# Optimization experiments

Hardware: AMD Instinct MI355X
Metric: run time of the kernel (lower is better)

Reference implementation:

```python
import jax, jax.numpy as jnp
import numpy as np

# Static config matching init_kwargs
DIM, HEADS = 128, 4
WH, WW = 4, 32          # window size (h, w)
SH, SW = 2, 2           # shift size (h, w)
H, W, B = 64, 512, 8
N = WH * WW             # tokens per window = 128
HD = DIM // HEADS       # head dim = 32
SCALE = HD ** -0.5
NHW, NWW = H // WH, W // WW
NWIN = NHW * NWW


def _rel_pos_index():
    coords = np.stack(np.meshgrid(np.arange(WH), np.arange(WW), indexing='ij'))  # (2,WH,WW)
    flat = coords.reshape(2, -1)                      # (2,N)
    rel = (flat[:, :, None] - flat[:, None, :]).transpose(1, 2, 0)  # (N,N,2)
    rel[:, :, 0] += WH - 1
    rel[:, :, 1] += WW - 1
    rel[:, :, 0] *= 2 * WW - 1
    return rel.sum(-1)                                # (N,N) int


def _attn_mask():
    img = np.zeros((H, W))
    cnt = 0
    for h in (slice(0, -WH), slice(-WH, -SH), slice(-SH, None)):
        for w in (slice(0, -WW), slice(-WW, -SW), slice(-SW, None)):
            img[h, w] = cnt
            cnt += 1
    mw = img.reshape(NHW, WH, NWW, WW).transpose(0, 2, 1, 3).reshape(-1, N)  # (nW,N)
    diff = mw[:, None, :] - mw[:, :, None]            # (nW,N,N)
    return np.where(diff != 0, -100.0, 0.0).astype(np.float32)


_RPI = _rel_pos_index()
_MASK = _attn_mask()


def _layernorm(x, g, b):
    m = jnp.mean(x, axis=-1, keepdims=True)
    v = jnp.mean(jnp.square(x - m), axis=-1, keepdims=True)
    return (x - m) * jax.lax.rsqrt(v + 1e-5) * g + b


def setup_inputs() -> dict:
    key = jax.random.key(0)
    ks = jax.random.split(key, 6)
    s = 0.02
    return {
        'x': jax.random.normal(ks[0], (B, H, W, DIM), jnp.float32),
        'g1': jnp.ones((DIM,), jnp.float32),
        'b1': jnp.zeros((DIM,), jnp.float32),
        'qkv_w': jax.random.normal(ks[1], (DIM, 3 * DIM), jnp.float32) * s,
        'qkv_b': jnp.zeros((3 * DIM,), jnp.float32),
        'rpb': jax.random.normal(ks[2], ((2 * WH - 1) * (2 * WW - 1), HEADS), jnp.float32) * s,
        'proj_w': jax.random.normal(ks[3], (DIM, DIM), jnp.float32) * s,
        'proj_b': jnp.zeros((DIM,), jnp.float32),
        'g2': jnp.ones((DIM,), jnp.float32),
        'b2': jnp.zeros((DIM,), jnp.float32),
        'fc1_w': jax.random.normal(ks[4], (DIM, 4 * DIM), jnp.float32) * s,
        'fc1_b': jnp.zeros((4 * DIM,), jnp.float32),
        'fc2_w': jax.random.normal(ks[5], (4 * DIM, DIM), jnp.float32) * s,
        'fc2_b': jnp.zeros((DIM,), jnp.float32),
    }


def reference(x, g1, b1, qkv_w, qkv_b, rpb, proj_w, proj_b, g2, b2,
              fc1_w, fc1_b, fc2_w, fc2_b):
    mask = jnp.asarray(_MASK)                         # (nW,N,N)
    # ---- W-MSA branch ----
    y = _layernorm(x, g1, b1)
    y = jnp.roll(y, (-SH, -SW), axis=(1, 2))          # cyclic shift
    # window partition: (B,H,W,C) -> (B*nW, N, C)
    xw = y.reshape(B, NHW, WH, NWW, WW, DIM).transpose(0, 1, 3, 2, 4, 5)
    xw = xw.reshape(B * NWIN, N, DIM)
    qkv = (xw @ qkv_w + qkv_b).reshape(B * NWIN, N, 3, HEADS, HD)
    qkv = qkv.transpose(2, 0, 3, 1, 4)                # (3, B_, h, N, d)
    q, k, v = qkv[0] * SCALE, qkv[1], qkv[2]
    attn = jnp.einsum('bhid,bhjd->bhij', q, k)        # (B_, h, N, N)
    bias = rpb[_RPI.reshape(-1)].reshape(N, N, HEADS).transpose(2, 0, 1)
    attn = attn + bias[None]
    attn = attn.reshape(B, NWIN, HEADS, N, N) + mask[None, :, None]
    attn = jax.nn.softmax(attn.reshape(B * NWIN, HEADS, N, N), axis=-1)
    o = jnp.einsum('bhij,bhjd->bhid', attn, v)        # (B_, h, N, d)
    o = o.transpose(0, 2, 1, 3).reshape(B * NWIN, N, DIM)
    o = o @ proj_w + proj_b
    # window reverse + reverse shift
    o = o.reshape(B, NHW, NWW, WH, WW, DIM).transpose(0, 1, 3, 2, 4, 5)
    o = o.reshape(B, H, W, DIM)
    o = jnp.roll(o, (SH, SW), axis=(1, 2))
    x = x + o
    # ---- MLP branch ----
    z = _layernorm(x, g2, b2)
    z = jax.nn.gelu(z @ fc1_w + fc1_b, approximate=False) @ fc2_w + fc2_b
    return x + z
```

## Files before the change

kernel.cpp:

```cpp
#include <hip/hip_runtime.h>
#include <hip/hip_bf16.h>
#include <math.h>

constexpr int BATCH = 8;
constexpr int IMG_H = 64;
constexpr int IMG_W = 512;
constexpr int DIM   = 128;
constexpr int WIN_H = 4, WIN_W = 32;
constexpr int SHIFT_H = 2, SHIFT_W = 2;
constexpr int NTOK = 128;
constexpr int HEADS = 4, HD = 32;
constexpr float QK_SCALE = 0.17677669529663687f;

typedef __attribute__((ext_vector_type(8))) short bf16x8;
typedef __attribute__((ext_vector_type(4))) float f32x4;

__device__ __forceinline__ unsigned short f2bf(float f) {
    unsigned u = __float_as_uint(f);
    u = (u + 0x7fffu + ((u >> 16) & 1u)) >> 16;
    return (unsigned short)u;
}

__device__ __forceinline__ int sc(int r, int c) {
    return (r << 7) + (c ^ ((r & 7) << 3));
}

__device__ __forceinline__ float gelu_tanh(float v) {
    const float u = v * (0.7978845608028654f + 0.035677408136300125f * v * v);
    const float e = exp2f(u * -2.8853900817779268f);
    return v * __builtin_amdgcn_rcpf(1.0f + e);
}

__global__ __launch_bounds__(256) void prep_weights(
    const float* __restrict__ fc1_w, const float* __restrict__ fc2_w,
    const float* __restrict__ qkv_w, const float* __restrict__ proj_w,
    unsigned short* __restrict__ w1t, unsigned short* __restrict__ w2t,
    unsigned short* __restrict__ qkv_wt, unsigned short* __restrict__ proj_wt)
{
    const int tid = blockIdx.x * 256 + threadIdx.x;
    if (tid < 512 * 128) {
        const int n = tid >> 7, k = tid & 127;
        w1t[tid] = f2bf(fc1_w[k * 512 + n]);
    } else if (tid < 2 * 512 * 128) {
        const int t = tid - 512 * 128;
        const int n = t >> 9, k = t & 511;
        w2t[t] = f2bf(fc2_w[k * 128 + n]);
    } else if (tid < 2 * 512 * 128 + 384 * 128) {
        const int t = tid - 2 * 512 * 128;
        const int n = t >> 7, k = t & 127;
        float v = qkv_w[k * 384 + n];
        if (n < 128) v *= QK_SCALE;
        qkv_wt[t] = f2bf(v);
    } else if (tid < 2 * 512 * 128 + 384 * 128 + 128 * 128) {
        const int t = tid - (2 * 512 * 128 + 384 * 128);
        const int n = t >> 7, k = t & 127;
        proj_wt[t] = f2bf(proj_w[k * 128 + n]);
    }
}

__global__ __launch_bounds__(512, 2) void swin_attn_mfma(
    const float* __restrict__ x,
    const float* __restrict__ g1,
    const float* __restrict__ b1,
    const unsigned short* __restrict__ qkv_wt,
    const float* __restrict__ qkv_b,
    const float* __restrict__ rpb,
    const unsigned short* __restrict__ proj_wt,
    const float* __restrict__ proj_b,
    float* __restrict__ out)
{
    __shared__ __align__(16) unsigned short s_xw[128 * 128];
    __shared__ __align__(16) unsigned short s_q [128 * 128];
    __shared__ __align__(16) unsigned short s_k [128 * 128];
    __shared__ __align__(16) unsigned short s_vt[128 * 128];
    __shared__ float s_rpb[441 * 4];

    const int tid = threadIdx.x;
    const int wv  = tid >> 6;
    const int ln  = tid & 63;
    const int g   = ln >> 4;
    const int c15 = ln & 15;
    const int kq  = g * 8;
    const int qr0 = wv * 16;

    const int b   = blockIdx.x >> 8;
    const int wid = blockIdx.x & 255;
    const int wp  = wid >> 4;
    const int wq  = wid & 15;

    {
        const int lh = ln & 31;
        const int hf = ln >> 5;
        const float4 gv = *(const float4*)&g1[lh * 4];
        const float4 bv = *(const float4*)&b1[lh * 4];
        #pragma unroll
        for (int it = 0; it < 8; ++it) {
            const int t  = qr0 + it * 2 + hf;
            const int th = t >> 5, tw = t & 31;
            const int gh = (wp * WIN_H + th + SHIFT_H) & (IMG_H - 1);
            const int gw = (wq * WIN_W + tw + SHIFT_W) & (IMG_W - 1);
            const float4 v = *(const float4*)&x[((((size_t)b * IMG_H + gh) * IMG_W + gw) * DIM) + lh * 4];
            float s  = v.x + v.y + v.z + v.w;
            float s2 = v.x * v.x + v.y * v.y + v.z * v.z + v.w * v.w;
            #pragma unroll
            for (int off = 1; off < 32; off <<= 1) {
                s  += __shfl_xor(s, off);
                s2 += __shfl_xor(s2, off);
            }
            const float mean = s * (1.0f / 128.0f);
            const float rs   = rsqrtf(s2 * (1.0f / 128.0f) - mean * mean + 1e-5f);
            const unsigned short o0 = f2bf((v.x - mean) * rs * gv.x + bv.x);
            const unsigned short o1 = f2bf((v.y - mean) * rs * gv.y + bv.y);
            const unsigned short o2 = f2bf((v.z - mean) * rs * gv.z + bv.z);
            const unsigned short o3 = f2bf((v.w - mean) * rs * gv.w + bv.w);
            uint2 pk;
            pk.x = (unsigned)o0 | ((unsigned)o1 << 16);
            pk.y = (unsigned)o2 | ((unsigned)o3 << 16);
            *(uint2*)&s_xw[sc(t, lh * 4)] = pk;
        }
    }

    for (int i = tid; i < 441 * 4; i += 512) s_rpb[i] = rpb[i];

    {
        bf16x8 afr[4];
        #pragma unroll
        for (int ks = 0; ks < 4; ++ks)
            afr[ks] = *(const bf16x8*)&s_xw[sc(qr0 + c15, ks * 32 + kq)];

        bf16x8 bfr[4];
        #pragma unroll
        for (int ks = 0; ks < 4; ++ks)
            bfr[ks] = *(const bf16x8*)&qkv_wt[(size_t)c15 * 128 + ks * 32 + kq];
        float bias = qkv_b[c15] * QK_SCALE;

        for (int ct = 0; ct < 24; ++ct) {
            const int ctn = (ct < 23) ? ct + 1 : 0;
            const int nn  = ctn * 16 + c15;
            bf16x8 bnx[4];
            #pragma unroll
            for (int ks = 0; ks < 4; ++ks)
                bnx[ks] = *(const bf16x8*)&qkv_wt[(size_t)nn * 128 + ks * 32 + kq];
            const float biasn = qkv_b[nn] * ((ctn < 8) ? QK_SCALE : 1.0f);

            f32x4 ac = (f32x4){0.f, 0.f, 0.f, 0.f};
            #pragma unroll
            for (int ks = 0; ks < 4; ++ks)
                ac = __builtin_amdgcn_mfma_f32_16x16x32_bf16(afr[ks], bfr[ks], ac, 0, 0, 0);

            const int part = ct >> 3;
            const int dc   = (ct & 7) * 16;
            #pragma unroll
            for (int r = 0; r < 4; ++r) {
                const int t = qr0 + g * 4 + r;
                const unsigned short hv = f2bf(ac[r] + bias);
                if (part == 0)      s_q [sc(t, dc + c15)] = hv;
                else if (part == 1) s_k [sc(t, dc + c15)] = hv;
                else                s_vt[sc(dc + c15, t)] = hv;
            }
            #pragma unroll
            for (int ks = 0; ks < 4; ++ks) bfr[ks] = bnx[ks];
            bias = biasn;
        }
    }

    __syncthreads();

    int colterm[8], rgj[8];
    #pragma unroll
    for (int jt = 0; jt < 8; ++jt) {
        const int j  = jt * 16 + c15;
        const int jh = j >> 5, jw = j & 31;
        colterm[jt] = jh * 63 + jw;
        const int gh1 = wp * WIN_H + jh, gw1 = wq * WIN_W + jw;
        rgj[jt] = ((gh1 < IMG_H - WIN_H) ? 0 : (gh1 < IMG_H - SHIFT_H ? 1 : 2)) * 3
                + ((gw1 < IMG_W - WIN_W) ? 0 : (gw1 < IMG_W - SHIFT_W ? 1 : 2));
    }

    f32x4 acc_out[8];
    #pragma unroll
    for (int n = 0; n < 8; ++n) acc_out[n] = (f32x4){0.f, 0.f, 0.f, 0.f};

    for (int h = 0; h < 4; ++h) {
        bf16x8 bk[8];
        #pragma unroll
        for (int jt = 0; jt < 8; ++jt)
            bk[jt] = *(const bf16x8*)&s_k[sc(jt * 16 + c15, h * 32 + kq)];

        const bf16x8 aq = *(const bf16x8*)&s_q[sc(qr0 + c15, h * 32 + kq)];
        f32x4 sacc[8];
        #pragma unroll
        for (int jt = 0; jt < 8; ++jt)
            sacc[jt] = __builtin_amdgcn_mfma_f32_16x16x32_bf16(
                aq, bk[jt], (f32x4){0.f, 0.f, 0.f, 0.f}, 0, 0, 0);

        #pragma unroll
        for (int r = 0; r < 4; ++r) {
            const int q  = qr0 + g * 4 + r;
            const int qh = q >> 5, qw = q & 31;
            const int rowterm = (qh + 3) * 63 + qw + 31;
            const int gh0 = wp * WIN_H + qh, gw0 = wq * WIN_W + qw;
            const int rgq = ((gh0 < IMG_H - WIN_H) ? 0 : (gh0 < IMG_H - SHIFT_H ? 1 : 2)) * 3
                          + ((gw0 < IMG_W - WIN_W) ? 0 : (gw0 < IMG_W - SHIFT_W ? 1 : 2));
            float vals[8];
            float mx = -1e30f;
            #pragma unroll
            for (int jt = 0; jt < 8; ++jt) {
                float a = sacc[jt][r] + s_rpb[(rowterm - colterm[jt]) * 4 + h];
                a = (rgj[jt] != rgq) ? a - 100.f : a;
                vals[jt] = a;
                mx = fmaxf(mx, a);
            }
            #pragma unroll
            for (int off = 1; off < 16; off <<= 1) mx = fmaxf(mx, __shfl_xor(mx, off));
            float den = 0.f;
            #pragma unroll
            for (int jt = 0; jt < 8; ++jt) {
                vals[jt] = exp2f((vals[jt] - mx) * 1.44269504f);
                den += vals[jt];
            }
            #pragma unroll
            for (int off = 1; off < 16; off <<= 1) den += __shfl_xor(den, off);
            const float inv = 1.0f / den;
            #pragma unroll
            for (int jt = 0; jt < 8; ++jt)
                s_xw[sc(q, jt * 16 + c15)] = f2bf(vals[jt] * inv);
        }

        f32x4 ao[2];
        ao[0] = (f32x4){0.f, 0.f, 0.f, 0.f};
        ao[1] = (f32x4){0.f, 0.f, 0.f, 0.f};
        #pragma unroll
        for (int ks = 0; ks < 4; ++ks) {
            const bf16x8 ap  = *(const bf16x8*)&s_xw[sc(qr0 + c15, ks * 32 + kq)];
            const bf16x8 bv0 = *(const bf16x8*)&s_vt[sc(h * 32 + c15,      ks * 32 + kq)];
            const bf16x8 bv1 = *(const bf16x8*)&s_vt[sc(h * 32 + 16 + c15, ks * 32 + kq)];
            ao[0] = __builtin_amdgcn_mfma_f32_16x16x32_bf16(ap, bv0, ao[0], 0, 0, 0);
            ao[1] = __builtin_amdgcn_mfma_f32_16x16x32_bf16(ap, bv1, ao[1], 0, 0, 0);
        }

        #pragma unroll
        for (int ct2 = 0; ct2 < 2; ++ct2)
            #pragma unroll
            for (int r = 0; r < 4; ++r)
                s_xw[sc(qr0 + g * 4 + r, ct2 * 16 + c15)] = f2bf(ao[ct2][r]);

        const bf16x8 aO = *(const bf16x8*)&s_xw[sc(qr0 + c15, kq)];
        #pragma unroll
        for (int ct8 = 0; ct8 < 8; ++ct8) {
            const bf16x8 bw = *(const bf16x8*)&proj_wt[(size_t)(ct8 * 16 + c15) * 128 + h * 32 + kq];
            acc_out[ct8] = __builtin_amdgcn_mfma_f32_16x16x32_bf16(aO, bw, acc_out[ct8], 0, 0, 0);
        }
    }

    #pragma unroll
    for (int ct8 = 0; ct8 < 8; ++ct8) {
        const float pb = proj_b[ct8 * 16 + c15];
        #pragma unroll
        for (int r = 0; r < 4; ++r) {
            const int t  = qr0 + g * 4 + r;
            const int th = t >> 5, tw = t & 31;
            const int gh = (wp * WIN_H + th + SHIFT_H) & (IMG_H - 1);
            const int gw = (wq * WIN_W + tw + SHIFT_W) & (IMG_W - 1);
            const size_t gi = (((size_t)b * IMG_H + gh) * IMG_W + gw) * DIM + ct8 * 16 + c15;
            out[gi] = x[gi] + acc_out[ct8][r] + pb;
        }
    }
}

__global__ __launch_bounds__(256) void swin_mlp_mfma(
    const float* __restrict__ g2, const float* __restrict__ beta2,
    const unsigned short* __restrict__ w1t,
    const float* __restrict__ fc1_b,
    const unsigned short* __restrict__ w2t,
    const float* __restrict__ fc2_b,
    float* __restrict__ out)
{
    __shared__ __align__(16) unsigned short s_x[64][136];
    __shared__ __align__(16) unsigned short s_h[64][72];
    __shared__ __align__(16) unsigned short s_w1[64][136];
    __shared__ __align__(16) unsigned short s_w2[128][72];

    const int tid = threadIdx.x;
    const int wv  = tid >> 6;
    const int ln  = tid & 63;
    const int m0  = wv * 16;
    const size_t tok0 = (size_t)blockIdx.x * 64;

    {
        const int lh = ln & 31;
        const int hf = ln >> 5;
        const float4 gv = *(const float4*)&g2[lh * 4];
        const float4 bv = *(const float4*)&beta2[lh * 4];
        for (int it = 0; it < 8; ++it) {
            const int t = m0 + it * 2 + hf;
            const float4 v = *(const float4*)&out[(tok0 + t) * 128 + lh * 4];
            float s  = v.x + v.y + v.z + v.w;
            float s2 = v.x * v.x + v.y * v.y + v.z * v.z + v.w * v.w;
            #pragma unroll
            for (int off = 1; off < 32; off <<= 1) {
                s  += __shfl_xor(s, off);
                s2 += __shfl_xor(s2, off);
            }
            const float mean = s * (1.0f / 128.0f);
            const float var  = s2 * (1.0f / 128.0f) - mean * mean;
            const float rs   = rsqrtf(var + 1e-5f);
            const unsigned short o0 = f2bf((v.x - mean) * rs * gv.x + bv.x);
            const unsigned short o1 = f2bf((v.y - mean) * rs * gv.y + bv.y);
            const unsigned short o2 = f2bf((v.z - mean) * rs * gv.z + bv.z);
            const unsigned short o3 = f2bf((v.w - mean) * rs * gv.w + bv.w);
            uint2 pk;
            pk.x = (unsigned)o0 | ((unsigned)o1 << 16);
            pk.y = (unsigned)o2 | ((unsigned)o3 << 16);
            *(uint2*)&s_x[t][lh * 4] = pk;
        }
    }

    f32x4 acc_o[8];
    #pragma unroll
    for (int i = 0; i < 8; ++i) acc_o[i] = (f32x4){0.f, 0.f, 0.f, 0.f};

    const int ar = m0 + (ln & 15);
    const int nr = ln & 15;
    const int kq = (ln >> 4) * 8;
    const int dr = m0 + (ln >> 4) * 4;

    for (int c = 0; c < 8; ++c) {
        for (int j = tid; j < 1024; j += 256) {
            const int row = j >> 4, c8 = j & 15;
            *(uint4*)&s_w1[row][c8 * 8] = *(const uint4*)&w1t[(size_t)(c * 64 + row) * 128 + c8 * 8];
        }
        for (int j = tid; j < 1024; j += 256) {
            const int row = j >> 3, c8 = j & 7;
            *(uint4*)&s_w2[row][c8 * 8] = *(const uint4*)&w2t[(size_t)row * 512 + c * 64 + c8 * 8];
        }
        __syncthreads();
        f32x4 hA[4];
        #pragma unroll
        for (int i = 0; i < 4; ++i) hA[i] = (f32x4){0.f, 0.f, 0.f, 0.f};
        #pragma unroll
        for (int ks = 0; ks < 4; ++ks) {
            const bf16x8 a = *(const bf16x8*)&s_x[ar][ks * 32 + kq];
            #pragma unroll
            for (int nt = 0; nt < 4; ++nt) {
                const bf16x8 bb = *(const bf16x8*)&s_w1[nt * 16 + nr][ks * 32 + kq];
                hA[nt] = __builtin_amdgcn_mfma_f32_16x16x32_bf16(a, bb, hA[nt], 0, 0, 0);
            }
        }
        #pragma unroll
        for (int nt = 0; nt < 4; ++nt) {
            const float bias = fc1_b[c * 64 + nt * 16 + nr];
            #pragma unroll
            for (int r = 0; r < 4; ++r) {
                const float v = hA[nt][r] + bias;
                s_h[dr + r][nt * 16 + nr] = f2bf(gelu_tanh(v));
            }
        }
        __syncthreads();
        #pragma unroll
        for (int ks = 0; ks < 2; ++ks) {
            const bf16x8 a = *(const bf16x8*)&s_h[ar][ks * 32 + kq];
            #pragma unroll
            for (int nt = 0; nt < 8; ++nt) {
                const bf16x8 bb = *(const bf16x8*)&s_w2[nt * 16 + nr][ks * 32 + kq];
                acc_o[nt] = __builtin_amdgcn_mfma_f32_16x16x32_bf16(a, bb, acc_o[nt], 0, 0, 0);
            }
        }
        __syncthreads();
    }

    #pragma unroll
    for (int nt = 0; nt < 8; ++nt) {
        const float bias = fc2_b[nt * 16 + nr];
        #pragma unroll
        for (int r = 0; r < 4; ++r) {
            const size_t gi = (tok0 + dr + r) * 128 + nt * 16 + nr;
            out[gi] = out[gi] + acc_o[nt][r] + bias;
        }
    }
}

extern "C" void kernel_launch(void* const* d_in, const int* in_sizes, int n_in,
                              void* d_out, int out_size, void* d_ws, size_t ws_size,
                              hipStream_t stream) {
    (void)in_sizes; (void)n_in; (void)out_size;
    const float* x      = (const float*)d_in[0];
    const float* g1     = (const float*)d_in[1];
    const float* b1     = (const float*)d_in[2];
    const float* qkv_w  = (const float*)d_in[3];
    const float* qkv_b  = (const float*)d_in[4];
    const float* rpb    = (const float*)d_in[5];
    const float* proj_w = (const float*)d_in[6];
    const float* proj_b = (const float*)d_in[7];
    const float* g2     = (const float*)d_in[8];
    const float* bb2    = (const float*)d_in[9];
    const float* fc1_w  = (const float*)d_in[10];
    const float* fc1_b  = (const float*)d_in[11];
    const float* fc2_w  = (const float*)d_in[12];
    const float* fc2_b  = (const float*)d_in[13];

    const size_t ws_needed = (size_t)(2 * 512 * 128 + 384 * 128 + 128 * 128)
                           * sizeof(unsigned short);
    if (ws_size != 0 && ws_size < ws_needed) {
        return;
    }

    unsigned short* w1t     = (unsigned short*)d_ws;
    unsigned short* w2t     = w1t + 512 * 128;
    unsigned short* qkv_wt  = w2t + 512 * 128;
    unsigned short* proj_wt = qkv_wt + 384 * 128;

    hipLaunchKernelGGL(prep_weights, dim3(768), dim3(256), 0, stream,
                       fc1_w, fc2_w, qkv_w, proj_w, w1t, w2t, qkv_wt, proj_wt);
    hipLaunchKernelGGL(swin_attn_mfma, dim3(BATCH * 256), dim3(512), 0, stream,
                       x, g1, b1, qkv_wt, qkv_b, rpb, proj_wt, proj_b, (float*)d_out);
    hipLaunchKernelGGL(swin_mlp_mfma, dim3(BATCH * IMG_H * IMG_W / 64), dim3(256), 0, stream,
                       g2, bb2, w1t, fc1_b, w2t, fc2_b, (float*)d_out);
}
```

Measured before the change: 838.3 us.

## Split MLP kernel N dimension across two waves per row group

The MLP kernel block grows from 256 to 512 threads. Each 16-row group is now handled by two waves, and each wave computes half of the fc1 hidden columns and half of the fc2 output columns. The LayerNorm prologue and the weight staging loops are redistributed over 512 threads. The aim is more waves per CU and less accumulator register pressure per wave, to better hide the LDS and global latency of the per-chunk weight loads. In exchange, each wave loads its A fragment twice as often relative to its MFMA work, and the blocks are larger.

```diff
diff --git a/kernel.cpp b/kernel.cpp
--- a/kernel.cpp
+++ b/kernel.cpp
@@ -268,7 +268,7 @@
     }
 }
 
-__global__ __launch_bounds__(256) void swin_mlp_mfma(
+__global__ __launch_bounds__(512, 4) void swin_mlp_mfma(
     const float* __restrict__ g2, const float* __restrict__ beta2,
     const unsigned short* __restrict__ w1t,
     const float* __restrict__ fc1_b,
@@ -284,16 +284,19 @@
     const int tid = threadIdx.x;
     const int wv  = tid >> 6;
     const int ln  = tid & 63;
-    const int m0  = wv * 16;
+    const int rg  = wv >> 1;
+    const int ch  = wv & 1;
+    const int m0  = rg * 16;
     const size_t tok0 = (size_t)blockIdx.x * 64;
 
     {
-        const int lh = ln & 31;
-        const int hf = ln >> 5;
+        const int lh = tid & 31;
+        const int hw = tid >> 5;
         const float4 gv = *(const float4*)&g2[lh * 4];
         const float4 bv = *(const float4*)&beta2[lh * 4];
-        for (int it = 0; it < 8; ++it) {
-            const int t = m0 + it * 2 + hf;
+        #pragma unroll
+        for (int it = 0; it < 4; ++it) {
+            const int t = it * 16 + hw;
             const float4 v = *(const float4*)&out[(tok0 + t) * 128 + lh * 4];
             float s  = v.x + v.y + v.z + v.w;
             float s2 = v.x * v.x + v.y * v.y + v.z * v.z + v.w * v.w;
@@ -303,8 +306,7 @@
                 s2 += __shfl_xor(s2, off);
             }
             const float mean = s * (1.0f / 128.0f);
-            const float var  = s2 * (1.0f / 128.0f) - mean * mean;
-            const float rs   = rsqrtf(var + 1e-5f);
+            const float rs   = rsqrtf(s2 * (1.0f / 128.0f) - mean * mean + 1e-5f);
             const unsigned short o0 = f2bf((v.x - mean) * rs * gv.x + bv.x);
             const unsigned short o1 = f2bf((v.y - mean) * rs * gv.y + bv.y);
             const unsigned short o2 = f2bf((v.z - mean) * rs * gv.z + bv.z);
@@ -316,9 +318,9 @@
         }
     }
 
-    f32x4 acc_o[8];
+    f32x4 acc_o[4];
     #pragma unroll
-    for (int i = 0; i < 8; ++i) acc_o[i] = (f32x4){0.f, 0.f, 0.f, 0.f};
+    for (int i = 0; i < 4; ++i) acc_o[i] = (f32x4){0.f, 0.f, 0.f, 0.f};
 
     const int ar = m0 + (ln & 15);
     const int nr = ln & 15;
@@ -326,33 +328,35 @@
     const int dr = m0 + (ln >> 4) * 4;
 
     for (int c = 0; c < 8; ++c) {
-        for (int j = tid; j < 1024; j += 256) {
+        for (int j = tid; j < 1024; j += 512) {
             const int row = j >> 4, c8 = j & 15;
             *(uint4*)&s_w1[row][c8 * 8] = *(const uint4*)&w1t[(size_t)(c * 64 + row) * 128 + c8 * 8];
         }
-        for (int j = tid; j < 1024; j += 256) {
+        for (int j = tid; j < 1024; j += 512) {
             const int row = j >> 3, c8 = j & 7;
             *(uint4*)&s_w2[row][c8 * 8] = *(const uint4*)&w2t[(size_t)row * 512 + c * 64 + c8 * 8];
         }
         __syncthreads();
-        f32x4 hA[4];
-        #pragma unroll
-        for (int i = 0; i < 4; ++i) hA[i] = (f32x4){0.f, 0.f, 0.f, 0.f};
+        f32x4 hA[2];
+        hA[0] = (f32x4){0.f, 0.f, 0.f, 0.f};
+        hA[1] = (f32x4){0.f, 0.f, 0.f, 0.f};
         #pragma unroll
         for (int ks = 0; ks < 4; ++ks) {
             const bf16x8 a = *(const bf16x8*)&s_x[ar][ks * 32 + kq];
             #pragma unroll
-            for (int nt = 0; nt < 4; ++nt) {
+            for (int n2 = 0; n2 < 2; ++n2) {
+                const int nt = ch * 2 + n2;
                 const bf16x8 bb = *(const bf16x8*)&s_w1[nt * 16 + nr][ks * 32 + kq];
-                hA[nt] = __builtin_amdgcn_mfma_f32_16x16x32_bf16(a, bb, hA[nt], 0, 0, 0);
-            }
-        }
-        #pragma unroll
-        for (int nt = 0; nt < 4; ++nt) {
+                hA[n2] = __builtin_amdgcn_mfma_f32_16x16x32_bf16(a, bb, hA[n2], 0, 0, 0);
+            }
+        }
+        #pragma unroll
+        for (int n2 = 0; n2 < 2; ++n2) {
+            const int nt = ch * 2 + n2;
             const float bias = fc1_b[c * 64 + nt * 16 + nr];
             #pragma unroll
             for (int r = 0; r < 4; ++r) {
-                const float v = hA[nt][r] + bias;
+                const float v = hA[n2][r] + bias;
                 s_h[dr + r][nt * 16 + nr] = f2bf(gelu_tanh(v));
             }
         }
@@ -361,21 +365,23 @@
         for (int ks = 0; ks < 2; ++ks) {
             const bf16x8 a = *(const bf16x8*)&s_h[ar][ks * 32 + kq];
             #pragma unroll
-            for (int nt = 0; nt < 8; ++nt) {
+            for (int n2 = 0; n2 < 4; ++n2) {
+                const int nt = ch * 4 + n2;
                 const bf16x8 bb = *(const bf16x8*)&s_w2[nt * 16 + nr][ks * 32 + kq];
-                acc_o[nt] = __builtin_amdgcn_mfma_f32_16x16x32_bf16(a, bb, acc_o[nt], 0, 0, 0);
+                acc_o[n2] = __builtin_amdgcn_mfma_f32_16x16x32_bf16(a, bb, acc_o[n2], 0, 0, 0);
             }
         }
         __syncthreads();
     }
 
     #pragma unroll
-    for (int nt = 0; nt < 8; ++nt) {
+    for (int n2 = 0; n2 < 4; ++n2) {
+        const int nt = ch * 4 + n2;
         const float bias = fc2_b[nt * 16 + nr];
         #pragma unroll
         for (int r = 0; r < 4; ++r) {
             const size_t gi = (tok0 + dr + r) * 128 + nt * 16 + nr;
-            out[gi] = out[gi] + acc_o[nt][r] + bias;
+            out[gi] = out[gi] + acc_o[n2][r] + bias;
         }
     }
 }
@@ -414,6 +420,6 @@
                        fc1_w, fc2_w, qkv_w, proj_w, w1t, w2t, qkv_wt, proj_wt);
     hipLaunchKernelGGL(swin_attn_mfma, dim3(BATCH * 256), dim3(512), 0, stream,
                        x, g1, b1, qkv_wt, qkv_b, rpb, proj_wt, proj_b, (float*)d_out);
-    hipLaunchKernelGGL(swin_mlp_mfma, dim3(BATCH * IMG_H * IMG_W / 64), dim3(256), 0, stream,
+    hipLaunchKernelGGL(swin_mlp_mfma, dim3(BATCH * IMG_H * IMG_W / 64), dim3(512), 0, stream,
                        g2, bb2, w1t, fc1_b, w2t, fc2_b, (float*)d_out);
 }
```

Result: faster. 738.3 us (-11.9%).
